# Kernel optimization log

Measured on AMD Instinct MI355X. Metric: run time of the kernel, lower is better.

The kernel has to match this reference:

```python
import jax, jax.numpy as jnp
import numpy as np

NUM_HEADS = 16
EPS = 1e-6
MAX_POS = 1000

def _pos_encoding(position, d):
    pos = np.arange(position)[:, None].astype(np.float32)
    i = np.arange(d)[None, :].astype(np.float32)
    angle = pos / np.power(10000.0, 2.0 * np.floor(i / 2.0) / np.float32(d))
    angle[:, 0::2] = np.sin(angle[:, 0::2])
    angle[:, 1::2] = np.cos(angle[:, 1::2])
    return jnp.asarray(angle[None], dtype=jnp.float32)  # [1, position, d]

def _layernorm(x, g, b):
    m = x.mean(-1, keepdims=True)
    v = ((x - m) ** 2).mean(-1, keepdims=True)
    return (x - m) * jax.lax.rsqrt(v + EPS) * g + b

def setup_inputs() -> dict:
    key = jax.random.key(0)
    L, D, F, B, S = 6, 1024, 4096, 4, 512
    sd = 0.02
    ks = jax.random.split(key, 8)
    return {
        "x": jax.random.normal(ks[0], (B, S, D), jnp.float32),
        "mask": jnp.zeros((B, 1, 1, S), jnp.float32),
        "Wq": sd * jax.random.normal(ks[1], (L, D, D), jnp.float32),
        "bq": jnp.zeros((L, D), jnp.float32),
        "Wk": sd * jax.random.normal(ks[2], (L, D, D), jnp.float32),
        "bk": jnp.zeros((L, D), jnp.float32),
        "Wv": sd * jax.random.normal(ks[3], (L, D, D), jnp.float32),
        "bv": jnp.zeros((L, D), jnp.float32),
        "Wo": sd * jax.random.normal(ks[4], (L, D, D), jnp.float32),
        "bo": jnp.zeros((L, D), jnp.float32),
        "W1": sd * jax.random.normal(ks[5], (L, D, F), jnp.float32),
        "b1": jnp.zeros((L, F), jnp.float32),
        "W2": sd * jax.random.normal(ks[6], (L, F, D), jnp.float32),
        "b2": jnp.zeros((L, D), jnp.float32),
        "g1": jnp.ones((L, D), jnp.float32),
        "be1": jnp.zeros((L, D), jnp.float32),
        "g2": jnp.ones((L, D), jnp.float32),
        "be2": jnp.zeros((L, D), jnp.float32),
    }

def reference(x, mask, Wq, bq, Wk, bk, Wv, bv, Wo, bo, W1, b1, W2, b2, g1, be1, g2, be2):
    B, S, D = x.shape
    H = NUM_HEADS
    depth = D // H
    scale = 1.0 / jnp.sqrt(jnp.float32(depth))
    x = x + _pos_encoding(MAX_POS, D)[:, :S, :]

    def layer(h, p):
        (wq, bq_, wk, bk_, wv, bv_, wo, bo_, w1, b1_, w2, b2_, g1_, be1_, g2_, be2_) = p
        split = lambda t: t.reshape(B, S, H, depth).transpose(0, 2, 1, 3)
        q = split(h @ wq + bq_)
        k = split(h @ wk + bk_)
        v = split(h @ wv + bv_)
        logits = jnp.einsum('bhqd,bhkd->bhqk', q, k) * scale + mask * (-1e9)
        a = jax.nn.softmax(logits, axis=-1)
        o = jnp.einsum('bhqk,bhkd->bhqd', a, v).transpose(0, 2, 1, 3).reshape(B, S, D)
        o = o @ wo + bo_
        h1 = _layernorm(h + o, g1_, be1_)
        f = jax.nn.relu(h1 @ w1 + b1_) @ w2 + b2_
        return _layernorm(h1 + f, g2_, be2_), None

    out, _ = jax.lax.scan(layer, x, (Wq, bq, Wk, bk, Wv, bv, Wo, bo, W1, b1, W2, b2, g1, be1, g2, be2))
    return out
```

## Files before the change

### kernel.cpp

```cpp
#include <hip/hip_runtime.h>

typedef __attribute__((ext_vector_type(8))) short bf16x8;
typedef __attribute__((ext_vector_type(4))) float f32x4;
typedef unsigned short u16;

#define D_MODEL 1024
#define SEQ 512
#define BATCH 4
#define NH 16
#define FF 4096
#define NLAYER 6
#define NTOKS 2048

__device__ __forceinline__ u16 f2bf(float f) {
  unsigned int u = __float_as_uint(f);
  u += 0x7fffu + ((u >> 16) & 1u);
  return (u16)(u >> 16);
}

__device__ __forceinline__ void gload16(const void* g, void* lds) {
  __builtin_amdgcn_global_load_lds((const __attribute__((address_space(1))) void*)g,
                                   (__attribute__((address_space(3))) void*)lds, 16, 0, 0);
}

__global__ __launch_bounds__(256) void posenc_k(const float* __restrict__ x, float* __restrict__ h,
                                                u16* __restrict__ hb) {
  int row = blockIdx.x;
  int s = row & (SEQ - 1);
  int t = threadIdx.x;
  float4 v = *(const float4*)(x + (size_t)row * D_MODEL + t * 4);
  float r[4] = {v.x, v.y, v.z, v.w};
#pragma unroll
  for (int j = 0; j < 4; ++j) {
    int d = t * 4 + j;
    int p = d >> 1;
    float ang = (float)s * exp2f((float)p * (-2.0f / 1024.0f) * 13.287712379549449f);
    r[j] += (d & 1) ? cosf(ang) : sinf(ang);
  }
  float4 o = {r[0], r[1], r[2], r[3]};
  *(float4*)(h + (size_t)row * D_MODEL + t * 4) = o;
  ushort4 ob;
  ob.x = f2bf(r[0]); ob.y = f2bf(r[1]); ob.z = f2bf(r[2]); ob.w = f2bf(r[3]);
  *(ushort4*)(hb + (size_t)row * D_MODEL + t * 4) = ob;
}

#define WTP 72
__device__ __forceinline__ void wconv_body(const float* __restrict__ src, u16* __restrict__ dst,
                                           int K, int N, float scale, int nb, int kb) {
  __shared__ u16 tile[64 * WTP];
  const int t = threadIdx.x;
#pragma unroll
  for (int rr = 0; rr < 4; ++rr) {
    int k = (t >> 4) + rr * 16;
    int n4 = (t & 15) * 4;
    float4 v = *(const float4*)(src + (size_t)(kb + k) * N + nb + n4);
    tile[(n4 + 0) * WTP + k] = f2bf(v.x * scale);
    tile[(n4 + 1) * WTP + k] = f2bf(v.y * scale);
    tile[(n4 + 2) * WTP + k] = f2bf(v.z * scale);
    tile[(n4 + 3) * WTP + k] = f2bf(v.w * scale);
  }
  __syncthreads();
#pragma unroll
  for (int rr = 0; rr < 2; ++rr) {
    int n = (t >> 3) + rr * 32;
    int kq = (t & 7) * 8;
    uint4 v = *(const uint4*)&tile[n * WTP + kq];
    *(uint4*)&dst[(size_t)(nb + n) * K + kb + kq] = v;
  }
}

__global__ __launch_bounds__(256) void wconv_qkv_k(const float* __restrict__ Wq,
                                                   const float* __restrict__ Wk,
                                                   const float* __restrict__ Wv,
                                                   u16* __restrict__ dst) {
  int z = blockIdx.z, l = z / 3, which = z % 3;
  const float* src = (which == 0 ? Wq : which == 1 ? Wk : Wv) + (size_t)l * 1024 * 1024;
  u16* d = dst + (size_t)l * 3072 * 1024 + (size_t)which * 1024 * 1024;
  float scale = (which == 0) ? 0.125f : 1.0f;
  wconv_body(src, d, 1024, 1024, scale, blockIdx.x * 64, blockIdx.y * 64);
}

__global__ __launch_bounds__(256) void wconv_gen_k(const float* __restrict__ W, u16* __restrict__ dst,
                                                   int K, int N) {
  int z = blockIdx.z;
  wconv_body(W + (size_t)z * K * N, dst + (size_t)z * N * K, K, N, 1.0f,
             blockIdx.x * 64, blockIdx.y * 64);
}

__global__ __launch_bounds__(256) void bqkv_k(const float* bq, const float* bk, const float* bv,
                                              float* o) {
  int i = blockIdx.x * 256 + threadIdx.x;
  int l = i / 3072, j = i % 3072;
  float v = (j < 1024) ? bq[l * 1024 + j] * 0.125f
                       : (j < 2048 ? bk[l * 1024 + j - 1024] : bv[l * 1024 + j - 2048]);
  o[i] = v;
}

template <int OBF, int RELU, int KSPLIT>
__global__ __launch_bounds__(256) void gemm128_k(const u16* __restrict__ A, const u16* __restrict__ Bt,
                                                 const float* __restrict__ bias, void* __restrict__ Cv,
                                                 int N, int K) {
  __shared__ u16 As[4][128 * 32];
  __shared__ u16 Bs[4][128 * 32];
  const int t = threadIdx.x, lane = t & 63, wave = t >> 6;
  const int wm = wave >> 1, wn = wave & 1;
  const int lrow = lane & 15, lgrp = lane >> 4;

  const int GX = N >> 7;
  const int nwg = GX * 16;
  int flat = blockIdx.y * GX + blockIdx.x;
  int q = nwg >> 3, r = nwg & 7, xcd = flat & 7, pos = flat >> 3;
  int logical = (xcd < r ? xcd * (q + 1) : r * (q + 1) + (xcd - r) * q) + pos;
  const int m0 = (logical & 15) * 128, n0 = (logical >> 4) * 128;

  const int kseg = K / KSPLIT;
  const int koff = (KSPLIT > 1) ? blockIdx.z * kseg : 0;

  f32x4 acc[4][4];
#pragma unroll
  for (int i = 0; i < 4; ++i)
#pragma unroll
    for (int j = 0; j < 4; ++j) acc[i][j] = (f32x4){0.f, 0.f, 0.f, 0.f};

  const u16* Ag = A + (size_t)m0 * K + koff;
  const u16* Bg = Bt + (size_t)n0 * K + koff;

  auto stage = [&](int buf, int k0) {
#pragma unroll
    for (int rr = 0; rr < 2; ++rr) {
      int s = rr * 256 + t;
      int row = s >> 2, cst = s & 3;
      int csrc = cst ^ ((row >> 1) & 3);
      gload16(Ag + (size_t)row * K + k0 + csrc * 8, &As[buf][s * 8]);
    }
#pragma unroll
    for (int rr = 0; rr < 2; ++rr) {
      int s = rr * 256 + t;
      int row = s >> 2, cst = s & 3;
      int csrc = cst ^ ((row >> 1) & 3);
      gload16(Bg + (size_t)row * K + k0 + csrc * 8, &Bs[buf][s * 8]);
    }
  };

  const int nk = kseg / 32;
  stage(0, 0);
  stage(1, 32);
  stage(2, 64);
  for (int tt = 0; tt < nk; ++tt) {
    if (tt + 2 < nk) asm volatile("s_waitcnt vmcnt(8)" ::: "memory");
    else if (tt + 1 < nk) asm volatile("s_waitcnt vmcnt(4)" ::: "memory");
    else asm volatile("s_waitcnt vmcnt(0)" ::: "memory");
    __builtin_amdgcn_s_barrier();
    __builtin_amdgcn_sched_barrier(0);
    if (tt + 3 < nk) stage((tt + 3) & 3, (tt + 3) * 32);
    const int cur = tt & 3;
    bf16x8 af[4], bfr[4];
#pragma unroll
    for (int i = 0; i < 4; ++i) {
      int row = wm * 64 + i * 16 + lrow;
      int sl = lgrp ^ ((row >> 1) & 3);
      af[i] = *(const bf16x8*)&As[cur][row * 32 + sl * 8];
    }
#pragma unroll
    for (int j = 0; j < 4; ++j) {
      int row = wn * 64 + j * 16 + lrow;
      int sl = lgrp ^ ((row >> 1) & 3);
      bfr[j] = *(const bf16x8*)&Bs[cur][row * 32 + sl * 8];
    }
    __builtin_amdgcn_s_setprio(1);
#pragma unroll
    for (int i = 0; i < 4; ++i)
#pragma unroll
      for (int j = 0; j < 4; ++j)
        acc[i][j] = __builtin_amdgcn_mfma_f32_16x16x32_bf16(af[i], bfr[j], acc[i][j], 0, 0, 0);
    __builtin_amdgcn_s_setprio(0);
  }

  const size_t outoff = (KSPLIT > 1) ? (size_t)blockIdx.z * NTOKS * N : 0;
#pragma unroll
  for (int j = 0; j < 4; ++j) {
    int col = n0 + wn * 64 + j * 16 + lrow;
    float bv = (KSPLIT == 1 || blockIdx.z == 0) ? bias[col] : 0.f;
#pragma unroll
    for (int i = 0; i < 4; ++i) {
      int rowb = m0 + wm * 64 + i * 16 + lgrp * 4;
#pragma unroll
      for (int r = 0; r < 4; ++r) {
        float v = acc[i][j][r] + bv;
        if (RELU) v = fmaxf(v, 0.f);
        if (OBF)
          ((u16*)Cv)[(size_t)(rowb + r) * N + col] = f2bf(v);
        else
          ((float*)Cv)[outoff + (size_t)(rowb + r) * N + col] = v;
      }
    }
  }
}

__global__ __launch_bounds__(256) void vtrans_k(const u16* __restrict__ qkv, u16* __restrict__ vt) {
  __shared__ u16 tile[32][33];
  const int bx = blockIdx.x, by = blockIdx.y, b = blockIdx.z;
  const int tx = threadIdx.x & 31, ty = threadIdx.x >> 5;
#pragma unroll
  for (int i = 0; i < 32; i += 8) {
    int sidx = bx * 32 + ty + i, d = by * 32 + tx;
    tile[ty + i][tx] = qkv[(size_t)(b * SEQ + sidx) * 3072 + 2048 + d];
  }
  __syncthreads();
#pragma unroll
  for (int i = 0; i < 32; i += 8) {
    int d = by * 32 + ty + i, sidx = bx * 32 + tx;
    vt[(size_t)(b * D_MODEL + d) * SEQ + sidx] = tile[tx][ty + i];
  }
}

#define KPAD 72
__global__ __launch_bounds__(256) void attn_k(const u16* __restrict__ qkv, const u16* __restrict__ vt,
                                              const float* __restrict__ mask, u16* __restrict__ o) {
  __shared__ u16 Ks[64 * KPAD];
  __shared__ u16 Vs[64 * KPAD];
  __shared__ u16 Ps[64 * KPAD];
  const int t = threadIdx.x;
  const int lane = t & 63, wave = t >> 6;
  const int lrow = lane & 15, lgrp = lane >> 4;
  const int qb = blockIdx.x;
  const int bh = blockIdx.y;
  const int b = bh >> 4, hh = bh & 15;

  bf16x8 qf[2];
  const int qrow0 = qb * 64 + wave * 16;
#pragma unroll
  for (int kk = 0; kk < 2; ++kk)
    qf[kk] = *(const bf16x8*)(qkv + (size_t)(b * SEQ + qrow0 + lrow) * 3072 +
                              hh * 64 + kk * 32 + lgrp * 8);

  float mreg[4], lsum[4];
  f32x4 oacc[4];
#pragma unroll
  for (int r = 0; r < 4; ++r) { mreg[r] = -1e30f; lsum[r] = 0.f; }
#pragma unroll
  for (int dn = 0; dn < 4; ++dn) oacc[dn] = (f32x4){0.f, 0.f, 0.f, 0.f};

  const int sr = t >> 3, sc = t & 7;
  for (int it = 0; it < 8; ++it) {
    const int kv0 = it * 64;
#pragma unroll
    for (int half = 0; half < 2; ++half) {
      int r = sr + half * 32;
      uint4 kv4 = *(const uint4*)(qkv + (size_t)(b * SEQ + kv0 + r) * 3072 + 1024 + hh * 64 + sc * 8);
      *(uint4*)(&Ks[r * KPAD + sc * 8]) = kv4;
      uint4 vv4 = *(const uint4*)(vt + (size_t)(bh * 64 + r) * SEQ + kv0 + sc * 8);
      *(uint4*)(&Vs[r * KPAD + sc * 8]) = vv4;
    }
    __syncthreads();

    f32x4 s[4];
#pragma unroll
    for (int nt = 0; nt < 4; ++nt) s[nt] = (f32x4){0.f, 0.f, 0.f, 0.f};
    __builtin_amdgcn_s_setprio(1);
#pragma unroll
    for (int nt = 0; nt < 4; ++nt)
#pragma unroll
      for (int kk = 0; kk < 2; ++kk) {
        bf16x8 kf = *(const bf16x8*)(&Ks[(nt * 16 + lrow) * KPAD + kk * 32 + lgrp * 8]);
        s[nt] = __builtin_amdgcn_mfma_f32_16x16x32_bf16(qf[kk], kf, s[nt], 0, 0, 0);
      }
    __builtin_amdgcn_s_setprio(0);
    float mv[4];
#pragma unroll
    for (int nt = 0; nt < 4; ++nt) mv[nt] = mask[b * SEQ + kv0 + nt * 16 + lrow] * -1e9f;
#pragma unroll
    for (int nt = 0; nt < 4; ++nt)
#pragma unroll
      for (int r = 0; r < 4; ++r) s[nt][r] = s[nt][r] + mv[nt];

#pragma unroll
    for (int r = 0; r < 4; ++r) {
      float mx = fmaxf(fmaxf(s[0][r], s[1][r]), fmaxf(s[2][r], s[3][r]));
      mx = fmaxf(mx, __shfl_xor(mx, 1));
      mx = fmaxf(mx, __shfl_xor(mx, 2));
      mx = fmaxf(mx, __shfl_xor(mx, 4));
      mx = fmaxf(mx, __shfl_xor(mx, 8));
      float mnew = fmaxf(mreg[r], mx);
      float corr = __expf(mreg[r] - mnew);
      mreg[r] = mnew;
      float p0 = __expf(s[0][r] - mnew);
      float p1 = __expf(s[1][r] - mnew);
      float p2 = __expf(s[2][r] - mnew);
      float p3 = __expf(s[3][r] - mnew);
      float rs = p0 + p1 + p2 + p3;
      rs += __shfl_xor(rs, 1);
      rs += __shfl_xor(rs, 2);
      rs += __shfl_xor(rs, 4);
      rs += __shfl_xor(rs, 8);
      lsum[r] = lsum[r] * corr + rs;
#pragma unroll
      for (int dn = 0; dn < 4; ++dn) oacc[dn][r] = oacc[dn][r] * corr;
      int prow = wave * 16 + lgrp * 4 + r;
      Ps[prow * KPAD + 0 + lrow] = f2bf(p0);
      Ps[prow * KPAD + 16 + lrow] = f2bf(p1);
      Ps[prow * KPAD + 32 + lrow] = f2bf(p2);
      Ps[prow * KPAD + 48 + lrow] = f2bf(p3);
    }
    __syncthreads();
    __builtin_amdgcn_s_setprio(1);
#pragma unroll
    for (int kk = 0; kk < 2; ++kk) {
      bf16x8 pf = *(const bf16x8*)(&Ps[(wave * 16 + lrow) * KPAD + kk * 32 + lgrp * 8]);
#pragma unroll
      for (int dn = 0; dn < 4; ++dn) {
        bf16x8 vf = *(const bf16x8*)(&Vs[(dn * 16 + lrow) * KPAD + kk * 32 + lgrp * 8]);
        oacc[dn] = __builtin_amdgcn_mfma_f32_16x16x32_bf16(pf, vf, oacc[dn], 0, 0, 0);
      }
    }
    __builtin_amdgcn_s_setprio(0);
    __syncthreads();
  }
#pragma unroll
  for (int dn = 0; dn < 4; ++dn)
#pragma unroll
    for (int r = 0; r < 4; ++r) {
      int qrow = qrow0 + lgrp * 4 + r;
      o[(size_t)(b * SEQ + qrow) * D_MODEL + hh * 64 + dn * 16 + lrow] =
          f2bf(oacc[dn][r] / lsum[r]);
    }
}

template <int P>
__global__ __launch_bounds__(256) void ln_k(const float* __restrict__ res, const float* __restrict__ parts,
                                            const float* __restrict__ g, const float* __restrict__ be,
                                            float* __restrict__ out, u16* __restrict__ outb) {
  __shared__ float red[8];
  const int row = blockIdx.x, t = threadIdx.x;
  float4 va = *(const float4*)(res + (size_t)row * D_MODEL + t * 4);
  float x0 = va.x, x1 = va.y, x2 = va.z, x3 = va.w;
#pragma unroll
  for (int p = 0; p < P; ++p) {
    float4 vp = *(const float4*)(parts + (size_t)p * NTOKS * D_MODEL + (size_t)row * D_MODEL + t * 4);
    x0 += vp.x; x1 += vp.y; x2 += vp.z; x3 += vp.w;
  }
  float s = x0 + x1 + x2 + x3;
  float s2 = x0 * x0 + x1 * x1 + x2 * x2 + x3 * x3;
#pragma unroll
  for (int off = 1; off < 64; off <<= 1) {
    s += __shfl_xor(s, off);
    s2 += __shfl_xor(s2, off);
  }
  const int wave = t >> 6, lane = t & 63;
  if (lane == 0) { red[wave] = s; red[4 + wave] = s2; }
  __syncthreads();
  s = red[0] + red[1] + red[2] + red[3];
  s2 = red[4] + red[5] + red[6] + red[7];
  float mean = s * (1.f / D_MODEL);
  float var = s2 * (1.f / D_MODEL) - mean * mean;
  float inv = rsqrtf(var + 1e-6f);
  float4 vg = *(const float4*)(g + t * 4);
  float4 ve = *(const float4*)(be + t * 4);
  float4 r;
  r.x = (x0 - mean) * inv * vg.x + ve.x;
  r.y = (x1 - mean) * inv * vg.y + ve.y;
  r.z = (x2 - mean) * inv * vg.z + ve.z;
  r.w = (x3 - mean) * inv * vg.w + ve.w;
  *(float4*)(out + (size_t)row * D_MODEL + t * 4) = r;
  if (outb) {
    ushort4 w;
    w.x = f2bf(r.x); w.y = f2bf(r.y); w.z = f2bf(r.z); w.w = f2bf(r.w);
    *(ushort4*)(outb + (size_t)row * D_MODEL + t * 4) = w;
  }
}

extern "C" void kernel_launch(void* const* d_in, const int* in_sizes, int n_in,
                              void* d_out, int out_size, void* d_ws, size_t ws_size,
                              hipStream_t stream) {
  const float* x = (const float*)d_in[0];
  const float* mask = (const float*)d_in[1];
  const float* Wq = (const float*)d_in[2];
  const float* bq = (const float*)d_in[3];
  const float* Wk = (const float*)d_in[4];
  const float* bk = (const float*)d_in[5];
  const float* Wv = (const float*)d_in[6];
  const float* bv = (const float*)d_in[7];
  const float* Wo = (const float*)d_in[8];
  const float* bo = (const float*)d_in[9];
  const float* W1 = (const float*)d_in[10];
  const float* b1 = (const float*)d_in[11];
  const float* W2 = (const float*)d_in[12];
  const float* b2 = (const float*)d_in[13];
  const float* g1 = (const float*)d_in[14];
  const float* be1 = (const float*)d_in[15];
  const float* g2 = (const float*)d_in[16];
  const float* be2 = (const float*)d_in[17];
  float* out = (float*)d_out;

  const size_t NTOK = (size_t)BATCH * SEQ;
  const size_t ACT = NTOK * D_MODEL;
  char* w = (char*)d_ws;
  float* h = (float*)w;     w += ACT * 4;
  float* h1 = (float*)w;    w += ACT * 4;
  float* op = (float*)w;    w += ACT * 4 * 4;
  u16* hb = (u16*)w;        w += ACT * 2;
  u16* h1b = (u16*)w;       w += ACT * 2;
  u16* qkvb = (u16*)w;      w += NTOK * 3072 * 2;
  u16* vt_ = (u16*)w;       w += ACT * 2;
  u16* obb = (u16*)w;       w += ACT * 2;
  u16* tb = (u16*)w;        w += NTOK * FF * 2;
  u16* wqkv_all = (u16*)w;  w += (size_t)NLAYER * 3072 * 1024 * 2;
  u16* wo_all = (u16*)w;    w += (size_t)NLAYER * 1024 * 1024 * 2;
  u16* w1_all = (u16*)w;    w += (size_t)NLAYER * 4096 * 1024 * 2;
  u16* w2_all = (u16*)w;    w += (size_t)NLAYER * 1024 * 4096 * 2;
  float* bqkv_all = (float*)w; w += (size_t)NLAYER * 3072 * 4;

  posenc_k<<<(int)NTOK, 256, 0, stream>>>(x, h, hb);
  wconv_qkv_k<<<dim3(16, 16, 18), 256, 0, stream>>>(Wq, Wk, Wv, wqkv_all);
  wconv_gen_k<<<dim3(16, 16, 6), 256, 0, stream>>>(Wo, wo_all, 1024, 1024);
  wconv_gen_k<<<dim3(64, 16, 6), 256, 0, stream>>>(W1, w1_all, 1024, 4096);
  wconv_gen_k<<<dim3(16, 64, 6), 256, 0, stream>>>(W2, w2_all, 4096, 1024);
  bqkv_k<<<72, 256, 0, stream>>>(bq, bk, bv, bqkv_all);

  for (int l = 0; l < NLAYER; ++l) {
    const u16* wqkv_t = wqkv_all + (size_t)l * 3072 * 1024;
    const u16* wo_t = wo_all + (size_t)l * 1024 * 1024;
    const u16* w1_t = w1_all + (size_t)l * 4096 * 1024;
    const u16* w2_t = w2_all + (size_t)l * 1024 * 4096;
    const float* bqkvl = bqkv_all + (size_t)l * 3072;
    const float* bol = bo + (size_t)l * D_MODEL;
    const float* b1l = b1 + (size_t)l * FF;
    const float* b2l = b2 + (size_t)l * D_MODEL;
    const float* g1l = g1 + (size_t)l * D_MODEL;
    const float* be1l = be1 + (size_t)l * D_MODEL;
    const float* g2l = g2 + (size_t)l * D_MODEL;
    const float* be2l = be2 + (size_t)l * D_MODEL;

    gemm128_k<1, 0, 1><<<dim3(24, 16), 256, 0, stream>>>(hb, wqkv_t, bqkvl, qkvb, 3072, 1024);
    vtrans_k<<<dim3(16, 32, 4), 256, 0, stream>>>(qkvb, vt_);
    attn_k<<<dim3(8, 64), 256, 0, stream>>>(qkvb, vt_, mask, obb);
    gemm128_k<0, 0, 4><<<dim3(8, 16, 4), 256, 0, stream>>>(obb, wo_t, bol, op, 1024, 1024);
    ln_k<4><<<(int)NTOK, 256, 0, stream>>>(h, op, g1l, be1l, h1, h1b);
    gemm128_k<1, 1, 1><<<dim3(32, 16), 256, 0, stream>>>(h1b, w1_t, b1l, tb, 4096, 1024);
    gemm128_k<0, 0, 4><<<dim3(8, 16, 4), 256, 0, stream>>>(tb, w2_t, b2l, op, 1024, 4096);
    ln_k<4><<<(int)NTOK, 256, 0, stream>>>(h1, op, g2l, be2l, (l == NLAYER - 1) ? out : h, hb);
  }
}
```

Baseline: 1.039 ms.

## Add 256x128 GEMM tile for FFN/out-proj and double-buffer K/V in attention

Adds a 512-thread GEMM kernel with 256x128 output tiles, a three-stage LDS pipeline and XCD-aware block remapping, and uses it for the output projection and both FFN GEMMs. The larger tile raises arithmetic intensity per block. Separately, the attention kernel now double-buffers K and V in shared memory, loading the next tile into registers while the current one is being computed, so global-load latency overlaps with the MFMA work. The cost is fewer blocks per launch, which can hurt occupancy on smaller GEMMs, plus higher LDS and register use in attention.

```diff
diff --git a/kernel.cpp b/kernel.cpp
--- a/kernel.cpp
+++ b/kernel.cpp
@@ -197,6 +197,105 @@
   }
 }
 
+template <int OBF, int RELU, int KSPLIT>
+__global__ __launch_bounds__(512) void gemm256_k(const u16* __restrict__ A, const u16* __restrict__ Bt,
+                                                 const float* __restrict__ bias, void* __restrict__ Cv,
+                                                 int N, int K) {
+  __shared__ u16 As[3][256 * 32];
+  __shared__ u16 Bs[3][128 * 32];
+  const int t = threadIdx.x, lane = t & 63, wave = t >> 6;
+  const int wm = wave >> 1, wn = wave & 1;
+  const int lrow = lane & 15, lgrp = lane >> 4;
+
+  const int GY = 8;
+  const int GX = N >> 7;
+  const int nwg = GX * GY;
+  int flat = blockIdx.y * GX + blockIdx.x;
+  int q = nwg >> 3, r = nwg & 7, xcd = flat & 7, pos = flat >> 3;
+  int logical = (xcd < r ? xcd * (q + 1) : r * (q + 1) + (xcd - r) * q) + pos;
+  const int m0 = (logical % GY) * 256, n0 = (logical / GY) * 128;
+
+  const int kseg = K / KSPLIT;
+  const int koff = (KSPLIT > 1) ? blockIdx.z * kseg : 0;
+
+  f32x4 acc[4][4];
+#pragma unroll
+  for (int i = 0; i < 4; ++i)
+#pragma unroll
+    for (int j = 0; j < 4; ++j) acc[i][j] = (f32x4){0.f, 0.f, 0.f, 0.f};
+
+  const u16* Ag = A + (size_t)m0 * K + koff;
+  const u16* Bg = Bt + (size_t)n0 * K + koff;
+
+  auto stage = [&](int buf, int k0) {
+#pragma unroll
+    for (int rr = 0; rr < 2; ++rr) {
+      int s = rr * 512 + t;
+      int row = s >> 2, cst = s & 3;
+      int csrc = cst ^ ((row >> 1) & 3);
+      gload16(Ag + (size_t)row * K + k0 + csrc * 8, &As[buf][s * 8]);
+    }
+    {
+      int s = t;
+      int row = s >> 2, cst = s & 3;
+      int csrc = cst ^ ((row >> 1) & 3);
+      gload16(Bg + (size_t)row * K + k0 + csrc * 8, &Bs[buf][s * 8]);
+    }
+  };
+
+  const int nk = kseg / 32;
+  stage(0, 0);
+  stage(1, 32);
+  for (int tt = 0; tt < nk; ++tt) {
+    if (tt + 1 < nk) asm volatile("s_waitcnt vmcnt(3)" ::: "memory");
+    else asm volatile("s_waitcnt vmcnt(0)" ::: "memory");
+    __builtin_amdgcn_s_barrier();
+    __builtin_amdgcn_sched_barrier(0);
+    if (tt + 2 < nk) stage((tt + 2) % 3, (tt + 2) * 32);
+    const int cur = tt % 3;
+    bf16x8 af[4], bfr[4];
+#pragma unroll
+    for (int i = 0; i < 4; ++i) {
+      int row = wm * 64 + i * 16 + lrow;
+      int sl = lgrp ^ ((row >> 1) & 3);
+      af[i] = *(const bf16x8*)&As[cur][row * 32 + sl * 8];
+    }
+#pragma unroll
+    for (int j = 0; j < 4; ++j) {
+      int row = wn * 64 + j * 16 + lrow;
+      int sl = lgrp ^ ((row >> 1) & 3);
+      bfr[j] = *(const bf16x8*)&Bs[cur][row * 32 + sl * 8];
+    }
+    __builtin_amdgcn_s_setprio(1);
+#pragma unroll
+    for (int i = 0; i < 4; ++i)
+#pragma unroll
+      for (int j = 0; j < 4; ++j)
+        acc[i][j] = __builtin_amdgcn_mfma_f32_16x16x32_bf16(af[i], bfr[j], acc[i][j], 0, 0, 0);
+    __builtin_amdgcn_s_setprio(0);
+  }
+
+  const size_t outoff = (KSPLIT > 1) ? (size_t)blockIdx.z * NTOKS * N : 0;
+#pragma unroll
+  for (int j = 0; j < 4; ++j) {
+    int col = n0 + wn * 64 + j * 16 + lrow;
+    float bv = (KSPLIT == 1 || blockIdx.z == 0) ? bias[col] : 0.f;
+#pragma unroll
+    for (int i = 0; i < 4; ++i) {
+      int rowb = m0 + wm * 64 + i * 16 + lgrp * 4;
+#pragma unroll
+      for (int r = 0; r < 4; ++r) {
+        float v = acc[i][j][r] + bv;
+        if (RELU) v = fmaxf(v, 0.f);
+        if (OBF)
+          ((u16*)Cv)[(size_t)(rowb + r) * N + col] = f2bf(v);
+        else
+          ((float*)Cv)[outoff + (size_t)(rowb + r) * N + col] = v;
+      }
+    }
+  }
+}
+
 __global__ __launch_bounds__(256) void vtrans_k(const u16* __restrict__ qkv, u16* __restrict__ vt) {
   __shared__ u16 tile[32][33];
   const int bx = blockIdx.x, by = blockIdx.y, b = blockIdx.z;
@@ -217,8 +316,8 @@
 #define KPAD 72
 __global__ __launch_bounds__(256) void attn_k(const u16* __restrict__ qkv, const u16* __restrict__ vt,
                                               const float* __restrict__ mask, u16* __restrict__ o) {
-  __shared__ u16 Ks[64 * KPAD];
-  __shared__ u16 Vs[64 * KPAD];
+  __shared__ u16 Ks[2][64 * KPAD];
+  __shared__ u16 Vs[2][64 * KPAD];
   __shared__ u16 Ps[64 * KPAD];
   const int t = threadIdx.x;
   const int lane = t & 63, wave = t >> 6;
@@ -242,17 +341,33 @@
   for (int dn = 0; dn < 4; ++dn) oacc[dn] = (f32x4){0.f, 0.f, 0.f, 0.f};
 
   const int sr = t >> 3, sc = t & 7;
+  uint4 kr[2], vr[2];
+#pragma unroll
+  for (int half = 0; half < 2; ++half) {
+    int r = sr + half * 32;
+    kr[half] = *(const uint4*)(qkv + (size_t)(b * SEQ + r) * 3072 + 1024 + hh * 64 + sc * 8);
+    vr[half] = *(const uint4*)(vt + (size_t)(bh * 64 + r) * SEQ + sc * 8);
+  }
+#pragma unroll
+  for (int half = 0; half < 2; ++half) {
+    int r = sr + half * 32;
+    *(uint4*)(&Ks[0][r * KPAD + sc * 8]) = kr[half];
+    *(uint4*)(&Vs[0][r * KPAD + sc * 8]) = vr[half];
+  }
+  __syncthreads();
+
   for (int it = 0; it < 8; ++it) {
+    const int cur = it & 1;
     const int kv0 = it * 64;
-#pragma unroll
-    for (int half = 0; half < 2; ++half) {
-      int r = sr + half * 32;
-      uint4 kv4 = *(const uint4*)(qkv + (size_t)(b * SEQ + kv0 + r) * 3072 + 1024 + hh * 64 + sc * 8);
-      *(uint4*)(&Ks[r * KPAD + sc * 8]) = kv4;
-      uint4 vv4 = *(const uint4*)(vt + (size_t)(bh * 64 + r) * SEQ + kv0 + sc * 8);
-      *(uint4*)(&Vs[r * KPAD + sc * 8]) = vv4;
-    }
-    __syncthreads();
+    if (it < 7) {
+      const int kv0n = kv0 + 64;
+#pragma unroll
+      for (int half = 0; half < 2; ++half) {
+        int r = sr + half * 32;
+        kr[half] = *(const uint4*)(qkv + (size_t)(b * SEQ + kv0n + r) * 3072 + 1024 + hh * 64 + sc * 8);
+        vr[half] = *(const uint4*)(vt + (size_t)(bh * 64 + r) * SEQ + kv0n + sc * 8);
+      }
+    }
 
     f32x4 s[4];
 #pragma unroll
@@ -262,7 +377,7 @@
     for (int nt = 0; nt < 4; ++nt)
 #pragma unroll
       for (int kk = 0; kk < 2; ++kk) {
-        bf16x8 kf = *(const bf16x8*)(&Ks[(nt * 16 + lrow) * KPAD + kk * 32 + lgrp * 8]);
+        bf16x8 kf = *(const bf16x8*)(&Ks[cur][(nt * 16 + lrow) * KPAD + kk * 32 + lgrp * 8]);
         s[nt] = __builtin_amdgcn_mfma_f32_16x16x32_bf16(qf[kk], kf, s[nt], 0, 0, 0);
       }
     __builtin_amdgcn_s_setprio(0);
@@ -309,11 +424,19 @@
       bf16x8 pf = *(const bf16x8*)(&Ps[(wave * 16 + lrow) * KPAD + kk * 32 + lgrp * 8]);
 #pragma unroll
       for (int dn = 0; dn < 4; ++dn) {
-        bf16x8 vf = *(const bf16x8*)(&Vs[(dn * 16 + lrow) * KPAD + kk * 32 + lgrp * 8]);
+        bf16x8 vf = *(const bf16x8*)(&Vs[cur][(dn * 16 + lrow) * KPAD + kk * 32 + lgrp * 8]);
         oacc[dn] = __builtin_amdgcn_mfma_f32_16x16x32_bf16(pf, vf, oacc[dn], 0, 0, 0);
       }
     }
     __builtin_amdgcn_s_setprio(0);
+    if (it < 7) {
+#pragma unroll
+      for (int half = 0; half < 2; ++half) {
+        int r = sr + half * 32;
+        *(uint4*)(&Ks[cur ^ 1][r * KPAD + sc * 8]) = kr[half];
+        *(uint4*)(&Vs[cur ^ 1][r * KPAD + sc * 8]) = vr[half];
+      }
+    }
     __syncthreads();
   }
 #pragma unroll
@@ -434,10 +557,10 @@
     gemm128_k<1, 0, 1><<<dim3(24, 16), 256, 0, stream>>>(hb, wqkv_t, bqkvl, qkvb, 3072, 1024);
     vtrans_k<<<dim3(16, 32, 4), 256, 0, stream>>>(qkvb, vt_);
     attn_k<<<dim3(8, 64), 256, 0, stream>>>(qkvb, vt_, mask, obb);
-    gemm128_k<0, 0, 4><<<dim3(8, 16, 4), 256, 0, stream>>>(obb, wo_t, bol, op, 1024, 1024);
+    gemm256_k<0, 0, 4><<<dim3(8, 8, 4), 512, 0, stream>>>(obb, wo_t, bol, op, 1024, 1024);
     ln_k<4><<<(int)NTOK, 256, 0, stream>>>(h, op, g1l, be1l, h1, h1b);
-    gemm128_k<1, 1, 1><<<dim3(32, 16), 256, 0, stream>>>(h1b, w1_t, b1l, tb, 4096, 1024);
-    gemm128_k<0, 0, 4><<<dim3(8, 16, 4), 256, 0, stream>>>(tb, w2_t, b2l, op, 1024, 4096);
+    gemm256_k<1, 1, 1><<<dim3(32, 8), 512, 0, stream>>>(h1b, w1_t, b1l, tb, 4096, 1024);
+    gemm256_k<0, 0, 4><<<dim3(8, 8, 4), 512, 0, stream>>>(tb, w2_t, b2l, op, 1024, 4096);
     ln_k<4><<<(int)NTOK, 256, 0, stream>>>(h1, op, g2l, be2l, (l == NLAYER - 1) ? out : h, hb);
   }
 }
```

Result: slower. 1.280 ms (+23.1%).

## Fuse V transpose into QKV GEMM epilogue and split attention over KV halves

Applied to the files above, without the earlier changes.

The QKV GEMM epilogue now writes the V columns directly in transposed layout, removing the separate transpose kernel. Attention is split across two KV halves via a third grid dimension, writing fp32 partial outputs plus running max and sum. A new combine kernel merges the halves with a log-sum-exp rescale and emits bf16. This doubles attention block count for better occupancy but adds partial-result traffic and an extra launch.

```diff
diff --git a/kernel.cpp b/kernel.cpp
--- a/kernel.cpp
+++ b/kernel.cpp
@@ -96,10 +96,10 @@
   o[i] = v;
 }
 
-template <int OBF, int RELU, int KSPLIT>
+template <int OBF, int RELU, int KSPLIT, int VTFUSE>
 __global__ __launch_bounds__(256) void gemm128_k(const u16* __restrict__ A, const u16* __restrict__ Bt,
                                                  const float* __restrict__ bias, void* __restrict__ Cv,
-                                                 int N, int K) {
+                                                 int N, int K, u16* __restrict__ vtout) {
   __shared__ u16 As[4][128 * 32];
   __shared__ u16 Bs[4][128 * 32];
   const int t = threadIdx.x, lane = t & 63, wave = t >> 6;
@@ -184,39 +184,34 @@
 #pragma unroll
     for (int i = 0; i < 4; ++i) {
       int rowb = m0 + wm * 64 + i * 16 + lgrp * 4;
-#pragma unroll
-      for (int r = 0; r < 4; ++r) {
-        float v = acc[i][j][r] + bv;
-        if (RELU) v = fmaxf(v, 0.f);
-        if (OBF)
-          ((u16*)Cv)[(size_t)(rowb + r) * N + col] = f2bf(v);
-        else
-          ((float*)Cv)[outoff + (size_t)(rowb + r) * N + col] = v;
+      if (VTFUSE && col >= 2048) {
+        int dg = col - 2048;
+        int bb = rowb >> 9, s0 = rowb & 511;
+        ushort4 wv;
+        wv.x = f2bf(acc[i][j][0] + bv);
+        wv.y = f2bf(acc[i][j][1] + bv);
+        wv.z = f2bf(acc[i][j][2] + bv);
+        wv.w = f2bf(acc[i][j][3] + bv);
+        *(ushort4*)&vtout[((size_t)(bb * 1024 + dg)) * 512 + s0] = wv;
+      } else {
+#pragma unroll
+        for (int r = 0; r < 4; ++r) {
+          float v = acc[i][j][r] + bv;
+          if (RELU) v = fmaxf(v, 0.f);
+          if (OBF)
+            ((u16*)Cv)[(size_t)(rowb + r) * N + col] = f2bf(v);
+          else
+            ((float*)Cv)[outoff + (size_t)(rowb + r) * N + col] = v;
+        }
       }
     }
-  }
-}
-
-__global__ __launch_bounds__(256) void vtrans_k(const u16* __restrict__ qkv, u16* __restrict__ vt) {
-  __shared__ u16 tile[32][33];
-  const int bx = blockIdx.x, by = blockIdx.y, b = blockIdx.z;
-  const int tx = threadIdx.x & 31, ty = threadIdx.x >> 5;
-#pragma unroll
-  for (int i = 0; i < 32; i += 8) {
-    int sidx = bx * 32 + ty + i, d = by * 32 + tx;
-    tile[ty + i][tx] = qkv[(size_t)(b * SEQ + sidx) * 3072 + 2048 + d];
-  }
-  __syncthreads();
-#pragma unroll
-  for (int i = 0; i < 32; i += 8) {
-    int d = by * 32 + ty + i, sidx = bx * 32 + tx;
-    vt[(size_t)(b * D_MODEL + d) * SEQ + sidx] = tile[tx][ty + i];
   }
 }
 
 #define KPAD 72
 __global__ __launch_bounds__(256) void attn_k(const u16* __restrict__ qkv, const u16* __restrict__ vt,
-                                              const float* __restrict__ mask, u16* __restrict__ o) {
+                                              const float* __restrict__ mask, float* __restrict__ opart,
+                                              float* __restrict__ ml) {
   __shared__ u16 Ks[64 * KPAD];
   __shared__ u16 Vs[64 * KPAD];
   __shared__ u16 Ps[64 * KPAD];
@@ -225,7 +220,9 @@
   const int lrow = lane & 15, lgrp = lane >> 4;
   const int qb = blockIdx.x;
   const int bh = blockIdx.y;
+  const int zz = blockIdx.z;
   const int b = bh >> 4, hh = bh & 15;
+  const int kvbase = zz * 256;
 
   bf16x8 qf[2];
   const int qrow0 = qb * 64 + wave * 16;
@@ -242,8 +239,8 @@
   for (int dn = 0; dn < 4; ++dn) oacc[dn] = (f32x4){0.f, 0.f, 0.f, 0.f};
 
   const int sr = t >> 3, sc = t & 7;
-  for (int it = 0; it < 8; ++it) {
-    const int kv0 = it * 64;
+  for (int it = 0; it < 4; ++it) {
+    const int kv0 = kvbase + it * 64;
 #pragma unroll
     for (int half = 0; half < 2; ++half) {
       int r = sr + half * 32;
@@ -316,14 +313,43 @@
     __builtin_amdgcn_s_setprio(0);
     __syncthreads();
   }
+  const size_t obase = (size_t)zz * NTOKS * D_MODEL;
 #pragma unroll
   for (int dn = 0; dn < 4; ++dn)
 #pragma unroll
     for (int r = 0; r < 4; ++r) {
       int qrow = qrow0 + lgrp * 4 + r;
-      o[(size_t)(b * SEQ + qrow) * D_MODEL + hh * 64 + dn * 16 + lrow] =
-          f2bf(oacc[dn][r] / lsum[r]);
-    }
+      opart[obase + (size_t)(b * SEQ + qrow) * D_MODEL + hh * 64 + dn * 16 + lrow] = oacc[dn][r];
+    }
+  if (lrow == 0) {
+#pragma unroll
+    for (int r = 0; r < 4; ++r) {
+      int qrow = qrow0 + lgrp * 4 + r;
+      float2 v = {mreg[r], lsum[r]};
+      ((float2*)ml)[((size_t)zz * NTOKS + b * SEQ + qrow) * NH + hh] = v;
+    }
+  }
+}
+
+__global__ __launch_bounds__(256) void acomb_k(const float* __restrict__ opart,
+                                               const float* __restrict__ ml,
+                                               u16* __restrict__ o) {
+  const int row = blockIdx.x, t = threadIdx.x;
+  const int head = t >> 4, col = head * 64 + (t & 15) * 4;
+  const float2* mlp = (const float2*)ml;
+  float2 a = mlp[(size_t)row * NH + head];
+  float2 b2 = mlp[((size_t)NTOKS + row) * NH + head];
+  float M = fmaxf(a.x, b2.x);
+  float w0 = __expf(a.x - M), w1 = __expf(b2.x - M);
+  float inv = 1.0f / (a.y * w0 + b2.y * w1);
+  float4 v0 = *(const float4*)(opart + (size_t)row * D_MODEL + col);
+  float4 v1 = *(const float4*)(opart + (size_t)(NTOKS + row) * D_MODEL + col);
+  ushort4 o4;
+  o4.x = f2bf((v0.x * w0 + v1.x * w1) * inv);
+  o4.y = f2bf((v0.y * w0 + v1.y * w1) * inv);
+  o4.z = f2bf((v0.z * w0 + v1.z * w1) * inv);
+  o4.w = f2bf((v0.w * w0 + v1.w * w1) * inv);
+  *(ushort4*)&o[(size_t)row * D_MODEL + col] = o4;
 }
 
 template <int P>
@@ -398,6 +424,8 @@
   float* h = (float*)w;     w += ACT * 4;
   float* h1 = (float*)w;    w += ACT * 4;
   float* op = (float*)w;    w += ACT * 4 * 4;
+  float* opart = (float*)w; w += ACT * 4 * 2;
+  float* mlbuf = (float*)w; w += (size_t)2 * NTOK * NH * 2 * 4;
   u16* hb = (u16*)w;        w += ACT * 2;
   u16* h1b = (u16*)w;       w += ACT * 2;
   u16* qkvb = (u16*)w;      w += NTOK * 3072 * 2;
@@ -431,13 +459,13 @@
     const float* g2l = g2 + (size_t)l * D_MODEL;
     const float* be2l = be2 + (size_t)l * D_MODEL;
 
-    gemm128_k<1, 0, 1><<<dim3(24, 16), 256, 0, stream>>>(hb, wqkv_t, bqkvl, qkvb, 3072, 1024);
-    vtrans_k<<<dim3(16, 32, 4), 256, 0, stream>>>(qkvb, vt_);
-    attn_k<<<dim3(8, 64), 256, 0, stream>>>(qkvb, vt_, mask, obb);
-    gemm128_k<0, 0, 4><<<dim3(8, 16, 4), 256, 0, stream>>>(obb, wo_t, bol, op, 1024, 1024);
+    gemm128_k<1, 0, 1, 1><<<dim3(24, 16), 256, 0, stream>>>(hb, wqkv_t, bqkvl, qkvb, 3072, 1024, vt_);
+    attn_k<<<dim3(8, 64, 2), 256, 0, stream>>>(qkvb, vt_, mask, opart, mlbuf);
+    acomb_k<<<(int)NTOK, 256, 0, stream>>>(opart, mlbuf, obb);
+    gemm128_k<0, 0, 4, 0><<<dim3(8, 16, 4), 256, 0, stream>>>(obb, wo_t, bol, op, 1024, 1024, nullptr);
     ln_k<4><<<(int)NTOK, 256, 0, stream>>>(h, op, g1l, be1l, h1, h1b);
-    gemm128_k<1, 1, 1><<<dim3(32, 16), 256, 0, stream>>>(h1b, w1_t, b1l, tb, 4096, 1024);
-    gemm128_k<0, 0, 4><<<dim3(8, 16, 4), 256, 0, stream>>>(tb, w2_t, b2l, op, 1024, 4096);
+    gemm128_k<1, 1, 1, 0><<<dim3(32, 16), 256, 0, stream>>>(h1b, w1_t, b1l, tb, 4096, 1024, nullptr);
+    gemm128_k<0, 0, 4, 0><<<dim3(8, 16, 4), 256, 0, stream>>>(tb, w2_t, b2l, op, 1024, 4096, nullptr);
     ln_k<4><<<(int)NTOK, 256, 0, stream>>>(h1, op, g2l, be2l, (l == NLAYER - 1) ? out : h, hb);
   }
 }
```

Result: no change. 1.054 ms (+1.4%).

## Fuse V transpose into QKV GEMM epilogue and store split-K partials as bf16

Applied to the files above, without the earlier changes.

The QKV GEMM epilogue now writes the V columns straight into the transposed vt buffer, which removes the separate vtrans kernel launch and its extra read and write pass. Split-K partial sums for the Wo and W2 GEMMs are stored as bf16 instead of fp32, and the layernorm kernel reads and widens them, which halves the partial-sum traffic. The cost is lower precision on the residual contributions, since each of the four partials is rounded to bf16. The V epilogue also issues scattered 8-byte stores along the sequence dimension.

```diff
diff --git a/kernel.cpp b/kernel.cpp
--- a/kernel.cpp
+++ b/kernel.cpp
@@ -16,6 +16,9 @@
   unsigned int u = __float_as_uint(f);
   u += 0x7fffu + ((u >> 16) & 1u);
   return (u16)(u >> 16);
+}
+__device__ __forceinline__ float bf2f(u16 v) {
+  return __uint_as_float(((unsigned int)v) << 16);
 }
 
 __device__ __forceinline__ void gload16(const void* g, void* lds) {
@@ -96,10 +99,10 @@
   o[i] = v;
 }
 
-template <int OBF, int RELU, int KSPLIT>
+template <int OBF, int RELU, int KSPLIT, int VTFUSE>
 __global__ __launch_bounds__(256) void gemm128_k(const u16* __restrict__ A, const u16* __restrict__ Bt,
                                                  const float* __restrict__ bias, void* __restrict__ Cv,
-                                                 int N, int K) {
+                                                 int N, int K, u16* __restrict__ vtout) {
   __shared__ u16 As[4][128 * 32];
   __shared__ u16 Bs[4][128 * 32];
   const int t = threadIdx.x, lane = t & 63, wave = t >> 6;
@@ -184,33 +187,31 @@
 #pragma unroll
     for (int i = 0; i < 4; ++i) {
       int rowb = m0 + wm * 64 + i * 16 + lgrp * 4;
-#pragma unroll
-      for (int r = 0; r < 4; ++r) {
-        float v = acc[i][j][r] + bv;
-        if (RELU) v = fmaxf(v, 0.f);
-        if (OBF)
-          ((u16*)Cv)[(size_t)(rowb + r) * N + col] = f2bf(v);
-        else
-          ((float*)Cv)[outoff + (size_t)(rowb + r) * N + col] = v;
+      if (VTFUSE && col >= 2048) {
+        int dg = col - 2048;
+        int bb = rowb >> 9, s0 = rowb & 511;
+        ushort4 wv;
+        wv.x = f2bf(acc[i][j][0] + bv);
+        wv.y = f2bf(acc[i][j][1] + bv);
+        wv.z = f2bf(acc[i][j][2] + bv);
+        wv.w = f2bf(acc[i][j][3] + bv);
+        *(ushort4*)&vtout[((size_t)(bb * 1024 + dg)) * 512 + s0] = wv;
+      } else if (KSPLIT > 1) {
+#pragma unroll
+        for (int r = 0; r < 4; ++r)
+          ((u16*)Cv)[outoff + (size_t)(rowb + r) * N + col] = f2bf(acc[i][j][r] + bv);
+      } else {
+#pragma unroll
+        for (int r = 0; r < 4; ++r) {
+          float v = acc[i][j][r] + bv;
+          if (RELU) v = fmaxf(v, 0.f);
+          if (OBF)
+            ((u16*)Cv)[(size_t)(rowb + r) * N + col] = f2bf(v);
+          else
+            ((float*)Cv)[(size_t)(rowb + r) * N + col] = v;
+        }
       }
     }
-  }
-}
-
-__global__ __launch_bounds__(256) void vtrans_k(const u16* __restrict__ qkv, u16* __restrict__ vt) {
-  __shared__ u16 tile[32][33];
-  const int bx = blockIdx.x, by = blockIdx.y, b = blockIdx.z;
-  const int tx = threadIdx.x & 31, ty = threadIdx.x >> 5;
-#pragma unroll
-  for (int i = 0; i < 32; i += 8) {
-    int sidx = bx * 32 + ty + i, d = by * 32 + tx;
-    tile[ty + i][tx] = qkv[(size_t)(b * SEQ + sidx) * 3072 + 2048 + d];
-  }
-  __syncthreads();
-#pragma unroll
-  for (int i = 0; i < 32; i += 8) {
-    int d = by * 32 + ty + i, sidx = bx * 32 + tx;
-    vt[(size_t)(b * D_MODEL + d) * SEQ + sidx] = tile[tx][ty + i];
   }
 }
 
@@ -327,7 +328,7 @@
 }
 
 template <int P>
-__global__ __launch_bounds__(256) void ln_k(const float* __restrict__ res, const float* __restrict__ parts,
+__global__ __launch_bounds__(256) void ln_k(const float* __restrict__ res, const u16* __restrict__ parts,
                                             const float* __restrict__ g, const float* __restrict__ be,
                                             float* __restrict__ out, u16* __restrict__ outb) {
   __shared__ float red[8];
@@ -336,8 +337,8 @@
   float x0 = va.x, x1 = va.y, x2 = va.z, x3 = va.w;
 #pragma unroll
   for (int p = 0; p < P; ++p) {
-    float4 vp = *(const float4*)(parts + (size_t)p * NTOKS * D_MODEL + (size_t)row * D_MODEL + t * 4);
-    x0 += vp.x; x1 += vp.y; x2 += vp.z; x3 += vp.w;
+    ushort4 vp = *(const ushort4*)(parts + (size_t)p * NTOKS * D_MODEL + (size_t)row * D_MODEL + t * 4);
+    x0 += bf2f(vp.x); x1 += bf2f(vp.y); x2 += bf2f(vp.z); x3 += bf2f(vp.w);
   }
   float s = x0 + x1 + x2 + x3;
   float s2 = x0 * x0 + x1 * x1 + x2 * x2 + x3 * x3;
@@ -397,7 +398,7 @@
   char* w = (char*)d_ws;
   float* h = (float*)w;     w += ACT * 4;
   float* h1 = (float*)w;    w += ACT * 4;
-  float* op = (float*)w;    w += ACT * 4 * 4;
+  u16* op = (u16*)w;        w += ACT * 2 * 4;
   u16* hb = (u16*)w;        w += ACT * 2;
   u16* h1b = (u16*)w;       w += ACT * 2;
   u16* qkvb = (u16*)w;      w += NTOK * 3072 * 2;
@@ -431,13 +432,12 @@
     const float* g2l = g2 + (size_t)l * D_MODEL;
     const float* be2l = be2 + (size_t)l * D_MODEL;
 
-    gemm128_k<1, 0, 1><<<dim3(24, 16), 256, 0, stream>>>(hb, wqkv_t, bqkvl, qkvb, 3072, 1024);
-    vtrans_k<<<dim3(16, 32, 4), 256, 0, stream>>>(qkvb, vt_);
+    gemm128_k<1, 0, 1, 1><<<dim3(24, 16), 256, 0, stream>>>(hb, wqkv_t, bqkvl, qkvb, 3072, 1024, vt_);
     attn_k<<<dim3(8, 64), 256, 0, stream>>>(qkvb, vt_, mask, obb);
-    gemm128_k<0, 0, 4><<<dim3(8, 16, 4), 256, 0, stream>>>(obb, wo_t, bol, op, 1024, 1024);
+    gemm128_k<0, 0, 4, 0><<<dim3(8, 16, 4), 256, 0, stream>>>(obb, wo_t, bol, op, 1024, 1024, nullptr);
     ln_k<4><<<(int)NTOK, 256, 0, stream>>>(h, op, g1l, be1l, h1, h1b);
-    gemm128_k<1, 1, 1><<<dim3(32, 16), 256, 0, stream>>>(h1b, w1_t, b1l, tb, 4096, 1024);
-    gemm128_k<0, 0, 4><<<dim3(8, 16, 4), 256, 0, stream>>>(tb, w2_t, b2l, op, 1024, 4096);
+    gemm128_k<1, 1, 1, 0><<<dim3(32, 16), 256, 0, stream>>>(h1b, w1_t, b1l, tb, 4096, 1024, nullptr);
+    gemm128_k<0, 0, 4, 0><<<dim3(8, 16, 4), 256, 0, stream>>>(tb, w2_t, b2l, op, 1024, 4096, nullptr);
     ln_k<4><<<(int)NTOK, 256, 0, stream>>>(h1, op, g2l, be2l, (l == NLAYER - 1) ? out : h, hb);
   }
 }
```

New measurement: 986.7 us. 1.05x faster.
